# Kernel optimization log

Measured on AMD Instinct MI355X. Metric: run time of the kernel, lower is better.

The kernel has to match this reference:

```python
import jax, jax.numpy as jnp
import numpy as np

B, N, D, H = 1, 4096, 768, 12
HD = D // H
SCALE = HD ** -0.5

def setup_inputs() -> dict:
    key = jax.random.key(0)
    k1, k2, k3 = jax.random.split(key, 3)
    x = jax.random.normal(k1, (B, N, D), dtype=jnp.float32)
    W_qkv = jax.random.normal(k2, (D, 3 * D), dtype=jnp.float32) * (D ** -0.5)
    W_out = jax.random.normal(k3, (D, D), dtype=jnp.float32) * (D ** -0.5)
    b_out = jnp.zeros((D,), dtype=jnp.float32)
    return {"x": x, "W_qkv": W_qkv, "W_out": W_out, "b_out": b_out}

def reference(x, W_qkv, W_out, b_out):
    # qkv projection: (B,N,3D)
    qkv = x @ W_qkv
    q, k, v = jnp.split(qkv, 3, axis=-1)
    # (B,N,D) -> (B,H,N,hd)
    def heads(t):
        return t.reshape(B, N, H, HD).transpose(0, 2, 1, 3)
    q, k, v = heads(q), heads(k), heads(v)
    scores = jnp.einsum('bhnd,bhmd->bhnm', q, k) * SCALE  # (B,H,N,N)
    attn = jax.nn.softmax(scores, axis=-1)
    out = jnp.einsum('bhnm,bhmd->bhnd', attn, v)
    out = out.transpose(0, 2, 1, 3).reshape(B, N, D)
    return out @ W_out + b_out
```

## Files before the change

### kernel.cpp

```cpp
#include <hip/hip_runtime.h>
#include <hip/hip_bf16.h>
#include <math.h>

typedef __attribute__((ext_vector_type(8))) short bf16x8;
typedef __attribute__((ext_vector_type(4))) short bf16x4;
typedef __attribute__((ext_vector_type(4))) float floatx4;
typedef __attribute__((ext_vector_type(4))) unsigned int uint4v;

constexpr int kN  = 4096;
constexpr int kD  = 768;
constexpr int kH  = 12;
constexpr int kHD = 64;
constexpr int k3D = 2304;
constexpr float kQScale = 0.18033688011112042f;

static __device__ __forceinline__ short f2b(float f) {
    __hip_bfloat16 h = __float2bfloat16(f);
    return *reinterpret_cast<short*>(&h);
}

static __device__ __forceinline__ float fast_exp2(float x) {
#if __has_builtin(__builtin_amdgcn_exp2f)
    return __builtin_amdgcn_exp2f(x);
#else
    return exp2f(x);
#endif
}

static __device__ __forceinline__ unsigned cvt_pk_bf16(float lo, float hi) {
    unsigned r;
    asm("v_cvt_pk_bf16_f32 %0, %1, %2" : "=v"(r) : "v"(lo), "v"(hi));
    return r;
}
static __device__ __forceinline__ void permlane32_swap(unsigned &a, unsigned &b) {
    asm("v_permlane32_swap_b32 %0, %1" : "+v"(a), "+v"(b));
}
static __device__ __forceinline__ void permlane16_swap(unsigned &a, unsigned &b) {
    asm("v_permlane16_swap_b32 %0, %1" : "+v"(a), "+v"(b));
}

static __device__ __forceinline__ void async_copy16(const void* g, void* l) {
    __builtin_amdgcn_global_load_lds(
        (const __attribute__((address_space(1))) void*)g,
        (__attribute__((address_space(3))) void*)l, 16, 0, 0);
}

constexpr int kBlkX  = 1536;
constexpr int kBlkWq = 72 * 24;
constexpr int kBlkWo = 24 * 24;

__global__ __launch_bounds__(256)
void prep(const float* __restrict__ x, const float* __restrict__ Wq,
          const float* __restrict__ Wo, short* __restrict__ Xb,
          short* __restrict__ WqT, short* __restrict__ WoT)
{
    const int bid = blockIdx.x;
    const int tid = threadIdx.x;
    if (bid < kBlkX) {
        const int i = bid * 256 + tid;
        const float4* s = reinterpret_cast<const float4*>(x + (size_t)i * 8);
        float4 a = s[0], b = s[1];
        bf16x8 v;
        v[0] = f2b(a.x); v[1] = f2b(a.y); v[2] = f2b(a.z); v[3] = f2b(a.w);
        v[4] = f2b(b.x); v[5] = f2b(b.y); v[6] = f2b(b.z); v[7] = f2b(b.w);
        *reinterpret_cast<bf16x8*>(Xb + (size_t)i * 8) = v;
        return;
    }
    const float* src; short* dst; int R, C, bx, by;
    if (bid < kBlkX + kBlkWq) {
        const int local = bid - kBlkX;
        src = Wq; dst = WqT; R = kD; C = k3D; bx = local % 72; by = local / 72;
    } else {
        const int local = bid - kBlkX - kBlkWq;
        src = Wo; dst = WoT; R = kD; C = kD; bx = local % 24; by = local / 24;
    }
    __shared__ float t[32][33];
    const int c0 = bx * 32, r0 = by * 32;
    const int tx = tid & 31, ty = tid >> 5;
    #pragma unroll
    for (int i = ty; i < 32; i += 8)
        t[i][tx] = src[(size_t)(r0 + i) * C + c0 + tx];
    __syncthreads();
    #pragma unroll
    for (int i = ty; i < 32; i += 8)
        dst[(size_t)(c0 + i) * R + r0 + tx] = f2b(t[tx][i]);
}

__global__ __launch_bounds__(256)
void gemm_qkv(const short* __restrict__ A, const short* __restrict__ BT,
              short* __restrict__ Qh, short* __restrict__ Kh, short* __restrict__ Vt)
{
    const int bm   = blockIdx.x * 128;
    const int bn   = blockIdx.y * 96;
    const int tid  = threadIdx.x;
    const int wave = tid >> 6;
    const int lane = tid & 63;
    const int l15  = lane & 15;
    const int quad = lane >> 4;
    const int l3   = l15 & 3;
    constexpr int K = kD;

    __shared__ alignas(16) short As[128 * 32];
    __shared__ alignas(16) short Bs[96 * 32];

    floatx4 acc[4][3] = {};
    const int wm = (wave >> 1) * 64;
    const int wn = (wave & 1) * 48;

    const bool vblk = (bn >= 2 * kD);

    const int srl = lane >> 2;
    const int scc = (lane & 3) ^ (srl & 3);

    for (int k0 = 0; k0 < K; k0 += 32) {
        __syncthreads();
        #pragma unroll
        for (int j = 0; j < 2; ++j) {
            const int rs = 32 * wave + 16 * j;
            async_copy16(&A[(size_t)(bm + rs + srl) * K + k0 + 8 * scc], &As[rs * 32]);
        }
        for (int rb = 16 * wave; rb < 96; rb += 64)
            async_copy16(&BT[(size_t)(bn + rb + srl) * K + k0 + 8 * scc], &Bs[rb * 32]);
        __syncthreads();

        bf16x8 af[4], bfr[3];
        #pragma unroll
        for (int mt = 0; mt < 4; ++mt)
            af[mt] = *reinterpret_cast<const bf16x8*>(&As[(wm + 16 * mt + l15) * 32 + 8 * (quad ^ l3)]);
        #pragma unroll
        for (int nt = 0; nt < 3; ++nt)
            bfr[nt] = *reinterpret_cast<const bf16x8*>(&Bs[(wn + 16 * nt + l15) * 32 + 8 * (quad ^ l3)]);
        if (vblk) {
            #pragma unroll
            for (int mt = 0; mt < 4; ++mt)
                #pragma unroll
                for (int nt = 0; nt < 3; ++nt)
                    acc[mt][nt] = __builtin_amdgcn_mfma_f32_16x16x32_bf16(bfr[nt], af[mt], acc[mt][nt], 0, 0, 0);
        } else {
            #pragma unroll
            for (int mt = 0; mt < 4; ++mt)
                #pragma unroll
                for (int nt = 0; nt < 3; ++nt)
                    acc[mt][nt] = __builtin_amdgcn_mfma_f32_16x16x32_bf16(af[mt], bfr[nt], acc[mt][nt], 0, 0, 0);
        }
    }

    if (vblk) {
        #pragma unroll
        for (int mt = 0; mt < 4; ++mt) {
            #pragma unroll
            for (int nt = 0; nt < 3; ++nt) {
                #pragma unroll
                for (int r = 0; r < 4; ++r) {
                    const int c      = bn + wn + nt * 16 + 4 * quad + r;
                    const int n      = bm + wm + mt * 16 + l15;
                    const int within = c - 2 * kD;
                    const int h = within >> 6;
                    const int d = within & 63;
                    Vt[((size_t)h * kHD + d) * kN + n] = f2b(acc[mt][nt][r]);
                }
            }
        }
        return;
    }

    #pragma unroll
    for (int mt = 0; mt < 4; ++mt) {
        #pragma unroll
        for (int nt = 0; nt < 3; ++nt) {
            #pragma unroll
            for (int r = 0; r < 4; ++r) {
                const int row = bm + wm + mt * 16 + 4 * quad + r;
                const int col = bn + wn + nt * 16 + l15;
                const float v = acc[mt][nt][r];
                const int proj   = col / kD;
                const int within = col - proj * kD;
                const int h = within >> 6;
                const int d = within & 63;
                if (proj == 0) Qh[((size_t)h * kN + row) * kHD + d] = f2b(v * kQScale);
                else           Kh[((size_t)h * kN + row) * kHD + d] = f2b(v);
            }
        }
    }
}

__global__ __launch_bounds__(256)
void gemm_out(const short* __restrict__ A, const short* __restrict__ BT,
              const float* __restrict__ bias, float* __restrict__ Cout)
{
    const int bm   = blockIdx.x * 64;
    const int bn   = blockIdx.y * 64;
    const int tid  = threadIdx.x;
    const int wave = tid >> 6;
    const int lane = tid & 63;
    const int l15  = lane & 15;
    const int quad = lane >> 4;
    const int l3   = l15 & 3;
    constexpr int K = kD;
    constexpr int N = kD;

    __shared__ alignas(16) short As[64 * 32];
    __shared__ alignas(16) short Bs[64 * 32];

    floatx4 acc[2][2] = {};
    const int wm = (wave >> 1) * 32;
    const int wn = (wave & 1) * 32;

    const int srl = lane >> 2;
    const int scc = (lane & 3) ^ (srl & 3);

    for (int k0 = 0; k0 < K; k0 += 32) {
        __syncthreads();
        const int rs = 16 * wave;
        async_copy16(&A [(size_t)(bm + rs + srl) * K + k0 + 8 * scc], &As[rs * 32]);
        async_copy16(&BT[(size_t)(bn + rs + srl) * K + k0 + 8 * scc], &Bs[rs * 32]);
        __syncthreads();

        bf16x8 af[2], bfr[2];
        #pragma unroll
        for (int mt = 0; mt < 2; ++mt)
            af[mt] = *reinterpret_cast<const bf16x8*>(&As[(wm + 16 * mt + l15) * 32 + 8 * (quad ^ l3)]);
        #pragma unroll
        for (int nt = 0; nt < 2; ++nt)
            bfr[nt] = *reinterpret_cast<const bf16x8*>(&Bs[(wn + 16 * nt + l15) * 32 + 8 * (quad ^ l3)]);
        #pragma unroll
        for (int mt = 0; mt < 2; ++mt)
            #pragma unroll
            for (int nt = 0; nt < 2; ++nt)
                acc[mt][nt] = __builtin_amdgcn_mfma_f32_16x16x32_bf16(af[mt], bfr[nt], acc[mt][nt], 0, 0, 0);
    }

    #pragma unroll
    for (int mt = 0; mt < 2; ++mt)
        #pragma unroll
        for (int nt = 0; nt < 2; ++nt)
            #pragma unroll
            for (int r = 0; r < 4; ++r) {
                const int row = bm + wm + mt * 16 + 4 * quad + r;
                const int col = bn + wn + nt * 16 + l15;
                Cout[(size_t)row * N + col] = acc[mt][nt][r] + bias[col];
            }
}

__global__ __launch_bounds__(256)
void attn(const short* __restrict__ Qh, const short* __restrict__ Kh,
          const short* __restrict__ Vt, short* __restrict__ AO)
{
    const int flat = blockIdx.y * 64 + blockIdx.x;
    const int W    = (flat & 7) * 96 + (flat >> 3);
    const int h    = W >> 6;
    const int q0   = (W & 63) * 64;

    const int tid  = threadIdx.x;
    const int wave = tid >> 6;
    const int lane = tid & 63;
    const int l15  = lane & 15;
    const int quad = lane >> 4;
    const int lx   = l15 & 7;
    const int wm   = wave >> 1;
    const int wk   = wave & 1;

    __shared__ alignas(16) short smem[16384];
    __shared__ float Dr[2][2][16];
    short* Ks0 = smem;
    short* Vs0 = smem + 8192;

    bf16x8 qf[2][2];
    {
        const size_t qb = ((size_t)h * kN + q0 + 32 * wm + l15) * kHD;
        #pragma unroll
        for (int mt = 0; mt < 2; ++mt)
            #pragma unroll
            for (int s = 0; s < 2; ++s)
                qf[mt][s] = *reinterpret_cast<const bf16x8*>(
                    &Qh[qb + (size_t)(16 * mt) * kHD + 32 * s + 8 * quad]);
    }

    bf16x8 onesf;
    #pragma unroll
    for (int i = 0; i < 8; ++i) onesf[i] = (short)0x3F80;

    floatx4 oacc[2][4] = {};
    floatx4 dacc[2] = {};

    const int srl = lane >> 3;
    const int scc = (lane & 7) ^ srl;

    const short* kgp = &Kh[(size_t)h * kN * kHD +
                           (size_t)(16 * wave + srl) * kHD + 8 * scc];
    const short* vgp = &Vt[(size_t)h * kHD * kN +
                           (size_t)(16 * wave + srl) * kN + 8 * scc];
    short* kls = Ks0 + (16 * wave) * 64;
    short* vls = Vs0 + (16 * wave) * 64;

    auto stage = [&](int b, int kv0) {
        #pragma unroll
        for (int j = 0; j < 2; ++j) {
            async_copy16(kgp + (size_t)(kv0 + 8 * j) * kHD, kls + b * 4096 + (8 * j) * 64);
            async_copy16(vgp + (size_t)(8 * j) * kN + kv0,  vls + b * 4096 + (8 * j) * 64);
        }
    };

    auto qk_exp = [&](const short* Kc, bf16x8 (&pa)[2]) {
        floatx4 sacc[2][2] = {};
        __builtin_amdgcn_s_setprio(1);
        #pragma unroll
        for (int nt = 0; nt < 2; ++nt) {
            #pragma unroll
            for (int s = 0; s < 2; ++s) {
                bf16x8 kf = *reinterpret_cast<const bf16x8*>(
                    &Kc[(32 * wk + 16 * nt + l15) * 64 + 8 * ((4 * s + quad) ^ lx)]);
                #pragma unroll
                for (int mt = 0; mt < 2; ++mt)
                    sacc[mt][nt] = __builtin_amdgcn_mfma_f32_16x16x32_bf16(
                        kf, qf[mt][s], sacc[mt][nt], 0, 0, 0);
            }
        }
        __builtin_amdgcn_s_setprio(0);
        #pragma unroll
        for (int mt = 0; mt < 2; ++mt) {
            float e[2][4];
            #pragma unroll
            for (int nt = 0; nt < 2; ++nt)
                #pragma unroll
                for (int r = 0; r < 4; ++r)
                    e[nt][r] = fast_exp2(sacc[mt][nt][r]);
            unsigned x0 = cvt_pk_bf16(e[0][0], e[0][1]);
            unsigned y0 = cvt_pk_bf16(e[1][0], e[1][1]);
            unsigned x1 = cvt_pk_bf16(e[0][2], e[0][3]);
            unsigned y1 = cvt_pk_bf16(e[1][2], e[1][3]);
            permlane32_swap(x0, y0);
            permlane16_swap(x0, y0);
            permlane32_swap(x1, y1);
            permlane16_swap(x1, y1);
            union { uint4v u; bf16x8 v; } pu;
            pu.u[0] = x0; pu.u[1] = x1; pu.u[2] = y0; pu.u[3] = y1;
            pa[mt] = pu.v;
        }
    };

    auto pv = [&](const short* Vc, const bf16x8 (&pa)[2]) {
        __builtin_amdgcn_s_setprio(1);
        #pragma unroll
        for (int dt = 0; dt < 4; ++dt) {
            bf16x8 vv = *reinterpret_cast<const bf16x8*>(
                &Vc[(16 * dt + l15) * 64 + 8 * ((4 * wk + quad) ^ lx)]);
            #pragma unroll
            for (int mt = 0; mt < 2; ++mt)
                oacc[mt][dt] = __builtin_amdgcn_mfma_f32_16x16x32_bf16(
                    pa[mt], vv, oacc[mt][dt], 0, 0, 0);
        }
        #pragma unroll
        for (int mt = 0; mt < 2; ++mt)
            dacc[mt] = __builtin_amdgcn_mfma_f32_16x16x32_bf16(
                pa[mt], onesf, dacc[mt], 0, 0, 0);
        __builtin_amdgcn_s_setprio(0);
    };

    constexpr int kNT = kN / 64;
    bf16x8 paA[2], paB[2];

    stage(0, 0);
    __syncthreads();
    stage(1, 64);
    qk_exp(Ks0, paA);
    int cur = 1;

    for (int tp = 0; tp < 31; ++tp) {
        const int u = 2 * tp + 1;
        pv(Vs0 + (cur ^ 1) * 4096, paA);
        __syncthreads();
        stage(cur ^ 1, (u + 1) * 64);
        qk_exp(Ks0 + cur * 4096, paB);
        cur ^= 1;
        pv(Vs0 + (cur ^ 1) * 4096, paB);
        __syncthreads();
        stage(cur ^ 1, (u + 2) * 64);
        qk_exp(Ks0 + cur * 4096, paA);
        cur ^= 1;
    }

    pv(Vs0 + (cur ^ 1) * 4096, paA);
    __syncthreads();
    qk_exp(Ks0 + cur * 4096, paB);
    pv(Vs0 + cur * 4096, paB);

    __syncthreads();
    float* red = reinterpret_cast<float*>(smem);
    if (wk == 1) {
        #pragma unroll
        for (int mt = 0; mt < 2; ++mt)
            #pragma unroll
            for (int dt = 0; dt < 4; ++dt)
                *reinterpret_cast<floatx4*>(
                    &red[wm * 2048 + (mt * 4 + dt) * 256 + l15 * 16 + quad * 4]) =
                    oacc[mt][dt];
        if (l15 == 0) {
            #pragma unroll
            for (int mt = 0; mt < 2; ++mt)
                #pragma unroll
                for (int r = 0; r < 4; ++r)
                    Dr[wm][mt][4 * quad + r] = dacc[mt][r];
        }
    }
    __syncthreads();
    if (wk == 0) {
        #pragma unroll
        for (int mt = 0; mt < 2; ++mt) {
            #pragma unroll
            for (int dt = 0; dt < 4; ++dt)
                oacc[mt][dt] += *reinterpret_cast<const floatx4*>(
                    &red[wm * 2048 + (mt * 4 + dt) * 256 + l15 * 16 + quad * 4]);
            float inv[4];
            #pragma unroll
            for (int r = 0; r < 4; ++r)
                inv[r] = 1.0f / (dacc[mt][r] + Dr[wm][mt][4 * quad + r]);
            #pragma unroll
            for (int dt = 0; dt < 4; ++dt) {
                #pragma unroll
                for (int r = 0; r < 4; ++r) {
                    const int row = q0 + 32 * wm + 16 * mt + 4 * quad + r;
                    const int col = h * kHD + 16 * dt + l15;
                    AO[(size_t)row * kD + col] = f2b(oacc[mt][dt][r] * inv[r]);
                }
            }
        }
    }
}

extern "C" void kernel_launch(void* const* d_in, const int* in_sizes, int n_in,
                              void* d_out, int out_size, void* d_ws, size_t ws_size,
                              hipStream_t stream)
{
    const float* x     = (const float*)d_in[0];
    const float* W_qkv = (const float*)d_in[1];
    const float* W_out = (const float*)d_in[2];
    const float* b_out = (const float*)d_in[3];
    float* out = (float*)d_out;

    const size_t HNHD = (size_t)kH * kN * kHD;
    short* Qh    = (short*)d_ws;
    short* Kh    = Qh + HNHD;
    short* Vt    = Kh + HNHD;
    short* Xb    = Vt + HNHD;
    short* WqkvT = Xb + (size_t)kN * kD;
    short* WoutT = WqkvT + (size_t)k3D * kD;
    short* AO    = Xb;
    (void)in_sizes; (void)n_in; (void)out_size; (void)ws_size;

    prep<<<dim3(kBlkX + kBlkWq + kBlkWo), dim3(256), 0, stream>>>(
        x, W_qkv, W_out, Xb, WqkvT, WoutT);

    gemm_qkv<<<dim3(kN / 128, k3D / 96), dim3(256), 0, stream>>>(
        Xb, WqkvT, Qh, Kh, Vt);
    attn<<<dim3(kN / 64, kH), dim3(256), 0, stream>>>(Qh, Kh, Vt, AO);
    gemm_out<<<dim3(kN / 64, kD / 64), dim3(256), 0, stream>>>(
        AO, WoutT, b_out, out);
}
```

Baseline: 200.1 us.

## Double-buffer LDS tiles in QKV and output projection GEMMs

Both projection GEMMs now use two shared-memory buffers, so async global-to-LDS copies for the next K tile are issued while MFMAs run on the current tile, and one of the two barriers per iteration is dropped. The output GEMM also widens its K tile from 32 to 64, using a new 8-way XOR swizzle that halves the number of loop iterations. The cost is doubled LDS use, which may lower occupancy, and these GEMMs are likely a minor part of total time next to attention.

```diff
diff --git a/kernel.cpp b/kernel.cpp
--- a/kernel.cpp
+++ b/kernel.cpp
@@ -100,8 +100,8 @@
     const int l3   = l15 & 3;
     constexpr int K = kD;
 
-    __shared__ alignas(16) short As[128 * 32];
-    __shared__ alignas(16) short Bs[96 * 32];
+    __shared__ alignas(16) short As[2][128 * 32];
+    __shared__ alignas(16) short Bs[2][96 * 32];
 
     floatx4 acc[4][3] = {};
     const int wm = (wave >> 1) * 64;
@@ -112,37 +112,51 @@
     const int srl = lane >> 2;
     const int scc = (lane & 3) ^ (srl & 3);
 
-    for (int k0 = 0; k0 < K; k0 += 32) {
-        __syncthreads();
+    auto stage = [&](int b, int k0) {
         #pragma unroll
         for (int j = 0; j < 2; ++j) {
             const int rs = 32 * wave + 16 * j;
-            async_copy16(&A[(size_t)(bm + rs + srl) * K + k0 + 8 * scc], &As[rs * 32]);
+            async_copy16(&A[(size_t)(bm + rs + srl) * K + k0 + 8 * scc], &As[b][rs * 32]);
         }
         for (int rb = 16 * wave; rb < 96; rb += 64)
-            async_copy16(&BT[(size_t)(bn + rb + srl) * K + k0 + 8 * scc], &Bs[rb * 32]);
+            async_copy16(&BT[(size_t)(bn + rb + srl) * K + k0 + 8 * scc], &Bs[b][rb * 32]);
+    };
+
+    constexpr int kNT = K / 32;
+    int cur = 0;
+    stage(0, 0);
+
+    for (int t = 0; t < kNT; ++t) {
         __syncthreads();
-
+        if (t + 1 < kNT) stage(cur ^ 1, (t + 1) * 32);
+
+        const short* Ac = As[cur];
+        const short* Bc = Bs[cur];
         bf16x8 af[4], bfr[3];
         #pragma unroll
         for (int mt = 0; mt < 4; ++mt)
-            af[mt] = *reinterpret_cast<const bf16x8*>(&As[(wm + 16 * mt + l15) * 32 + 8 * (quad ^ l3)]);
+            af[mt] = *reinterpret_cast<const bf16x8*>(
+                &Ac[(wm + 16 * mt + l15) * 32 + 8 * (quad ^ l3)]);
         #pragma unroll
         for (int nt = 0; nt < 3; ++nt)
-            bfr[nt] = *reinterpret_cast<const bf16x8*>(&Bs[(wn + 16 * nt + l15) * 32 + 8 * (quad ^ l3)]);
+            bfr[nt] = *reinterpret_cast<const bf16x8*>(
+                &Bc[(wn + 16 * nt + l15) * 32 + 8 * (quad ^ l3)]);
         if (vblk) {
             #pragma unroll
             for (int mt = 0; mt < 4; ++mt)
                 #pragma unroll
                 for (int nt = 0; nt < 3; ++nt)
-                    acc[mt][nt] = __builtin_amdgcn_mfma_f32_16x16x32_bf16(bfr[nt], af[mt], acc[mt][nt], 0, 0, 0);
+                    acc[mt][nt] = __builtin_amdgcn_mfma_f32_16x16x32_bf16(
+                        bfr[nt], af[mt], acc[mt][nt], 0, 0, 0);
         } else {
             #pragma unroll
             for (int mt = 0; mt < 4; ++mt)
                 #pragma unroll
                 for (int nt = 0; nt < 3; ++nt)
-                    acc[mt][nt] = __builtin_amdgcn_mfma_f32_16x16x32_bf16(af[mt], bfr[nt], acc[mt][nt], 0, 0, 0);
-        }
+                    acc[mt][nt] = __builtin_amdgcn_mfma_f32_16x16x32_bf16(
+                        af[mt], bfr[nt], acc[mt][nt], 0, 0, 0);
+        }
+        cur ^= 1;
     }
 
     if (vblk) {
@@ -195,39 +209,61 @@
     const int lane = tid & 63;
     const int l15  = lane & 15;
     const int quad = lane >> 4;
-    const int l3   = l15 & 3;
+    const int lx   = l15 & 7;
     constexpr int K = kD;
     constexpr int N = kD;
 
-    __shared__ alignas(16) short As[64 * 32];
-    __shared__ alignas(16) short Bs[64 * 32];
+    __shared__ alignas(16) short As[2][64 * 64];
+    __shared__ alignas(16) short Bs[2][64 * 64];
 
     floatx4 acc[2][2] = {};
     const int wm = (wave >> 1) * 32;
     const int wn = (wave & 1) * 32;
 
-    const int srl = lane >> 2;
-    const int scc = (lane & 3) ^ (srl & 3);
-
-    for (int k0 = 0; k0 < K; k0 += 32) {
+    const int srl = lane >> 3;
+    const int scc = (lane & 7) ^ srl;
+
+    auto stage = [&](int b, int k0) {
+        #pragma unroll
+        for (int j = 0; j < 2; ++j) {
+            const int rs = 16 * wave + 8 * j;
+            async_copy16(&A [(size_t)(bm + rs + srl) * K + k0 + 8 * scc], &As[b][rs * 64]);
+            async_copy16(&BT[(size_t)(bn + rs + srl) * K + k0 + 8 * scc], &Bs[b][rs * 64]);
+        }
+    };
+
+    constexpr int kNT = K / 64;
+    int cur = 0;
+    stage(0, 0);
+
+    for (int t = 0; t < kNT; ++t) {
         __syncthreads();
-        const int rs = 16 * wave;
-        async_copy16(&A [(size_t)(bm + rs + srl) * K + k0 + 8 * scc], &As[rs * 32]);
-        async_copy16(&BT[(size_t)(bn + rs + srl) * K + k0 + 8 * scc], &Bs[rs * 32]);
-        __syncthreads();
-
-        bf16x8 af[2], bfr[2];
+        if (t + 1 < kNT) stage(cur ^ 1, (t + 1) * 64);
+
+        const short* Ac = As[cur];
+        const short* Bc = Bs[cur];
+        bf16x8 af[2][2], bfr[2][2];
         #pragma unroll
         for (int mt = 0; mt < 2; ++mt)
-            af[mt] = *reinterpret_cast<const bf16x8*>(&As[(wm + 16 * mt + l15) * 32 + 8 * (quad ^ l3)]);
+            #pragma unroll
+            for (int s = 0; s < 2; ++s)
+                af[mt][s] = *reinterpret_cast<const bf16x8*>(
+                    &Ac[(wm + 16 * mt + l15) * 64 + 8 * ((4 * s + quad) ^ lx)]);
         #pragma unroll
         for (int nt = 0; nt < 2; ++nt)
-            bfr[nt] = *reinterpret_cast<const bf16x8*>(&Bs[(wn + 16 * nt + l15) * 32 + 8 * (quad ^ l3)]);
-        #pragma unroll
-        for (int mt = 0; mt < 2; ++mt)
-            #pragma unroll
-            for (int nt = 0; nt < 2; ++nt)
-                acc[mt][nt] = __builtin_amdgcn_mfma_f32_16x16x32_bf16(af[mt], bfr[nt], acc[mt][nt], 0, 0, 0);
+            #pragma unroll
+            for (int s = 0; s < 2; ++s)
+                bfr[nt][s] = *reinterpret_cast<const bf16x8*>(
+                    &Bc[(wn + 16 * nt + l15) * 64 + 8 * ((4 * s + quad) ^ lx)]);
+        #pragma unroll
+        for (int s = 0; s < 2; ++s)
+            #pragma unroll
+            for (int mt = 0; mt < 2; ++mt)
+                #pragma unroll
+                for (int nt = 0; nt < 2; ++nt)
+                    acc[mt][nt] = __builtin_amdgcn_mfma_f32_16x16x32_bf16(
+                        af[mt][s], bfr[nt][s], acc[mt][nt], 0, 0, 0);
+        cur ^= 1;
     }
 
     #pragma unroll
```

Measured after the change: 197.9 us. No clear change (-1.1%).
